# Kernel optimization log

Hardware: AMD Instinct MI355X
Metric: run time of the kernel (lower is better)

The kernel has to match this reference:

```python
import jax, jax.numpy as jnp
import numpy as np

ACTION_SCALE = 0.01
LOG_STD_MIN, LOG_STD_MAX = -20.0, 2.0


def setup_inputs() -> dict:
    key = jax.random.key(0)
    k1, k2, k3 = jax.random.split(key, 3)
    B, N, D = 8, 1024, 128
    kv = jax.random.normal(k1, (B, N, 4 * D), dtype=jnp.float32)
    positions = jax.random.normal(k2, (B, N, 3), dtype=jnp.float32)
    eps = jax.random.normal(k3, (B, N, 3), dtype=jnp.float32)  # standard-normal sample for rsample
    return {"kv": kv, "positions": positions, "eps": eps}


def reference(kv, positions, eps):
    # Split Atomwise output into mean/std key-value embeddings: each [B, N, D]
    k_mu, v_mu, k_sigma, v_sigma = jnp.split(kv, 4, axis=-1)

    # Low-rank attention-like pairwise scores: [B, N, N]
    rel_shifts_mean = jnp.einsum("bid,bjd->bij", k_mu, v_mu)
    rel_shifts_log_std = jnp.einsum("bid,bjd->bij", k_sigma, v_sigma)

    # All-pairs unit displacement vectors: [B, N, N, 3]
    P = positions[:, :, None, :] - positions[:, None, :, :]
    norm = jnp.linalg.norm(P, axis=-1) + 1e-8
    P = P / norm[..., None]

    # Weighted sum over the j axis (torch dim=-2): [B, N, 3]
    actions_mean = jnp.einsum("bijc,bij->bic", P, rel_shifts_mean)
    actions_log_std = jnp.clip(
        jnp.einsum("bijc,bij->bic", P, rel_shifts_log_std), LOG_STD_MIN, LOG_STD_MAX
    )
    actions_std = jnp.exp(actions_log_std)

    # TanhNormal rsample (training branch) with externally supplied noise eps
    pre_tanh = actions_mean + actions_std * eps
    actions = jnp.tanh(pre_tanh)

    # Normal log-prob minus tanh log-det-Jacobian
    normal_lp = (
        -0.5 * ((pre_tanh - actions_mean) / actions_std) ** 2
        - actions_log_std
        - 0.5 * jnp.log(2.0 * jnp.pi)
    )
    log_det = (
        2.0 * jnp.log(2.0)
        + jax.nn.log_sigmoid(2.0 * pre_tanh)
        + jax.nn.log_sigmoid(-2.0 * pre_tanh)
    )
    log_prob = jnp.sum(normal_lp - log_det, axis=(1, 2))[:, None]  # [B, 1]

    actions = actions * ACTION_SCALE
    # change-of-variables correction for the action_scale factor
    n_dims = pre_tanh.shape[1] * pre_tanh.shape[2]
    log_prob = log_prob - n_dims * jnp.log(ACTION_SCALE)
    return actions, log_prob
```

## Files before the change

### kernel.cpp

```cpp
#include <hip/hip_runtime.h>
#include <math.h>


#define NTOK 1024
#define LPCONST 14147.0828114f

typedef __bf16 bf16x8 __attribute__((ext_vector_type(8)));
typedef float f32x4 __attribute__((ext_vector_type(4)));
#define MFMA(a, b, c) __builtin_amdgcn_mfma_f32_16x16x32_bf16(a, b, c, 0, 0, 0)

__device__ __forceinline__ unsigned short to_bf16(float x) {
    return (unsigned short)((__float_as_uint(x) + 0x8000u) >> 16);
}

template <int CTRL>
__device__ __forceinline__ float dpp_add(float v) {
    int y = __builtin_amdgcn_update_dpp(0, __float_as_int(v), CTRL, 0xf, 0xf, true);
    return v + __int_as_float(y);
}
__device__ __forceinline__ float red16(float v) {
    v = dpp_add<0xB1>(v);
    v = dpp_add<0x4E>(v);
    v = dpp_add<0x141>(v);
    v = dpp_add<0x140>(v);
    return v;
}

__device__ __forceinline__ float softplusf(float z) {
    return z > 20.f ? z : log1pf(expf(z));
}

__global__ __launch_bounds__(256) void prepass_kernel(
    const float* __restrict__ kv, unsigned short* __restrict__ frag,
    float* __restrict__ out)
{
    const int t = blockIdx.x * 256 + threadIdx.x;
    if (t < 8) out[8 * NTOK * 3 + t] = LPCONST;

    const int lane = t & 63;
    const int kc   = (t >> 6) & 3;
    const int tile = (t >> 8) & 63;
    const int b    = (t >> 14) & 7;
    const int side = t >> 17;

    const int row = tile * 16 + (lane & 15);
    const int kof = kc * 32 + (lane >> 4) * 8;
    const float* gp = kv + ((size_t)b * NTOK + row) * 512 + side * 128 + kof;
    const float4 m0 = *(const float4*)gp;
    const float4 m1 = *(const float4*)(gp + 4);
    const float4 s0 = *(const float4*)(gp + 256);
    const float4 s1 = *(const float4*)(gp + 260);

    unsigned short* cp = frag + (size_t)side * 2097152 +
                         (size_t)(b * 64 + tile) * 4096 + kc * 1024 + lane * 8;
    ushort4 h0, h1;
    h0.x = to_bf16(m0.x); h0.y = to_bf16(m0.y); h0.z = to_bf16(m0.z); h0.w = to_bf16(m0.w);
    h1.x = to_bf16(m1.x); h1.y = to_bf16(m1.y); h1.z = to_bf16(m1.z); h1.w = to_bf16(m1.w);
    *(ushort4*)(cp + 0) = h0; *(ushort4*)(cp + 4) = h1;
    h0.x = to_bf16(s0.x); h0.y = to_bf16(s0.y); h0.z = to_bf16(s0.z); h0.w = to_bf16(s0.w);
    h1.x = to_bf16(s1.x); h1.y = to_bf16(s1.y); h1.z = to_bf16(s1.z); h1.w = to_bf16(s1.w);
    *(ushort4*)(cp + 512) = h0; *(ushort4*)(cp + 516) = h1;
}

__global__ __launch_bounds__(512) void actor_kernel(
    const unsigned short* __restrict__ frag, const float* __restrict__ pos,
    const float* __restrict__ eps, float* __restrict__ out)
{
    const int t = threadIdx.x;
    const int w = t >> 6;
    const int lane = t & 63;
    const int q = lane >> 4;
    const int r16 = lane & 15;
    const int b   = blockIdx.x & 7;
    const int itx = blockIdx.x >> 3;
    const int i0 = itx * 16;

    const unsigned short* fragK = frag;
    const unsigned short* fragV = frag + 2097152;
    const float* posb = pos + (size_t)b * NTOK * 3;

    __shared__ float spos[NTOK * 3];
    __shared__ float wacc[8 * 16 * 6];
    __shared__ float fin[96];

    #pragma unroll
    for (int u = t; u < 768; u += 512)
        *(float4*)&spos[u * 4] = *(const float4*)&posb[u * 4];

    const unsigned short* kp = fragK + (size_t)(b * 64 + itx) * 4096 + lane * 8;
    bf16x8 Km[4], Ks[4];
    #pragma unroll
    for (int kc = 0; kc < 4; ++kc) {
        Km[kc] = *(const bf16x8*)(kp + kc * 1024);
        Ks[kc] = *(const bf16x8*)(kp + kc * 1024 + 512);
    }

    __syncthreads();

    const int i = i0 + r16;
    const float pix = spos[i * 3 + 0];
    const float piy = spos[i * 3 + 1];
    const float piz = spos[i * 3 + 2];

    float am0 = 0.f, am1 = 0.f, am2 = 0.f;
    float al0 = 0.f, al1 = 0.f, al2 = 0.f;

    const unsigned short* vbase =
        fragV + (size_t)(b * 64 + w * 8) * 4096 + lane * 8;

    #pragma unroll 2
    for (int jt = 0; jt < 8; ++jt) {
        const unsigned short* vp = vbase + jt * 4096;
        f32x4 accm = (f32x4){0.f, 0.f, 0.f, 0.f};
        f32x4 accs = (f32x4){0.f, 0.f, 0.f, 0.f};
        #pragma unroll
        for (int kc = 0; kc < 4; ++kc) {
            const bf16x8 Vm = *(const bf16x8*)(vp + kc * 1024);
            const bf16x8 Vs = *(const bf16x8*)(vp + kc * 1024 + 512);
            accm = MFMA(Vm, Km[kc], accm);
            accs = MFMA(Vs, Ks[kc], accs);
        }
        const int jbase = (w * 8 + jt) * 16 + q * 4;
        #pragma unroll
        for (int reg = 0; reg < 4; ++reg) {
            const float* pj = &spos[(jbase + reg) * 3];
            const float dx = pix - pj[0];
            const float dy = piy - pj[1];
            const float dz = piz - pj[2];
            const float d2 = dx * dx + dy * dy + dz * dz;
            const float inv = d2 > 0.f ? rsqrtf(d2) : 0.f;
            const float wm = accm[reg] * inv;
            const float ws = accs[reg] * inv;
            am0 = fmaf(dx, wm, am0); am1 = fmaf(dy, wm, am1); am2 = fmaf(dz, wm, am2);
            al0 = fmaf(dx, ws, al0); al1 = fmaf(dy, ws, al1); al2 = fmaf(dz, ws, al2);
        }
    }

    am0 += __shfl_xor(am0, 16, 64); am0 += __shfl_xor(am0, 32, 64);
    am1 += __shfl_xor(am1, 16, 64); am1 += __shfl_xor(am1, 32, 64);
    am2 += __shfl_xor(am2, 16, 64); am2 += __shfl_xor(am2, 32, 64);
    al0 += __shfl_xor(al0, 16, 64); al0 += __shfl_xor(al0, 32, 64);
    al1 += __shfl_xor(al1, 16, 64); al1 += __shfl_xor(al1, 32, 64);
    al2 += __shfl_xor(al2, 16, 64); al2 += __shfl_xor(al2, 32, 64);

    if (lane < 16) {
        float* p = wacc + (w * 16 + r16) * 6;
        p[0] = am0; p[1] = am1; p[2] = am2; p[3] = al0; p[4] = al1; p[5] = al2;
    }
    __syncthreads();
    if (t < 96) {
        float v = 0.f;
        #pragma unroll
        for (int ww = 0; ww < 8; ++ww) v += wacc[ww * 96 + t];
        fin[t] = v;
    }
    __syncthreads();

    if (t < 16) {
        const int gi = b * NTOK + i0 + t;
        const float* v = fin + t * 6;
        float lp = 0.f;
        #pragma unroll
        for (int c = 0; c < 3; ++c) {
            const float als = fminf(fmaxf(v[3 + c], -20.f), 2.f);
            const float sd = expf(als);
            const float e = eps[gi * 3 + c];
            const float pre = fmaf(sd, e, v[c]);
            out[gi * 3 + c] = tanhf(pre) * 0.01f;
            const float t2 = 2.f * pre;
            lp += -0.5f * e * e - als - 2.3052328944f + softplusf(t2) + softplusf(-t2);
        }
        lp = red16(lp);
        if (t == 0) atomicAdd(out + 8 * NTOK * 3 + b, lp);
    }
}

extern "C" void kernel_launch(void* const* d_in, const int* in_sizes, int n_in,
                              void* d_out, int out_size, void* d_ws, size_t ws_size,
                              hipStream_t stream) {
    const float* kv = (const float*)d_in[0];
    const float* pos = (const float*)d_in[1];
    const float* eps = (const float*)d_in[2];
    float* out = (float*)d_out;
    unsigned short* frag = (unsigned short*)d_ws;

    prepass_kernel<<<dim3(1024), 256, 0, stream>>>(kv, frag, out);
    actor_kernel<<<dim3(512), 512, 0, stream>>>(frag, pos, eps, out);
}
```

Before: 92.72 us.

## Process two 16-row i-tiles per block, staging K fragments in LDS

Each block now handles 32 query rows (two MFMA i-tiles) with 1024 threads across 16 waves. Each V fragment loaded from global memory is reused for two K tiles, halving V traffic per output row, and the grid shrinks to 256 blocks. K fragments are staged in shared memory instead of registers. The trade-offs are fewer blocks than CUs on the device, repeated LDS reads of K inside the inner loop, and a larger cross-wave reduction.

```diff
diff --git a/kernel.cpp b/kernel.cpp
--- a/kernel.cpp
+++ b/kernel.cpp
@@ -62,7 +62,7 @@
     *(ushort4*)(cp + 512) = h0; *(ushort4*)(cp + 516) = h1;
 }
 
-__global__ __launch_bounds__(512) void actor_kernel(
+__global__ __launch_bounds__(1024) void actor_kernel(
     const unsigned short* __restrict__ frag, const float* __restrict__ pos,
     const float* __restrict__ eps, float* __restrict__ out)
 {
@@ -71,92 +71,127 @@
     const int lane = t & 63;
     const int q = lane >> 4;
     const int r16 = lane & 15;
-    const int b   = blockIdx.x & 7;
-    const int itx = blockIdx.x >> 3;
-    const int i0 = itx * 16;
+    const int b    = blockIdx.x & 7;
+    const int ithx = blockIdx.x >> 3;
+    const int i0 = ithx * 32;
 
     const unsigned short* fragK = frag;
     const unsigned short* fragV = frag + 2097152;
     const float* posb = pos + (size_t)b * NTOK * 3;
 
+    __shared__ unsigned short sK[8192];
     __shared__ float spos[NTOK * 3];
-    __shared__ float wacc[8 * 16 * 6];
-    __shared__ float fin[96];
+    __shared__ float wacc[16 * 32 * 6];
+    __shared__ float fin[192];
+
+    {
+        const unsigned short* kg =
+            fragK + (size_t)(b * 64 + ithx * 2) * 4096 + t * 8;
+        *(ushort4*)&sK[t * 8 + 0] = *(const ushort4*)(kg + 0);
+        *(ushort4*)&sK[t * 8 + 4] = *(const ushort4*)(kg + 4);
+    }
+    if (t < 768) *(float4*)&spos[t * 4] = *(const float4*)&posb[t * 4];
+    __syncthreads();
+
+    const float pix0 = spos[(i0 + r16) * 3 + 0];
+    const float piy0 = spos[(i0 + r16) * 3 + 1];
+    const float piz0 = spos[(i0 + r16) * 3 + 2];
+    const float pix1 = spos[(i0 + 16 + r16) * 3 + 0];
+    const float piy1 = spos[(i0 + 16 + r16) * 3 + 1];
+    const float piz1 = spos[(i0 + 16 + r16) * 3 + 2];
+
+    float am[2][3] = {};
+    float al[2][3] = {};
+
+    const unsigned short* vbase =
+        fragV + (size_t)(b * 64 + w * 4) * 4096 + lane * 8;
+    const int klofs = lane * 8;
 
     #pragma unroll
-    for (int u = t; u < 768; u += 512)
-        *(float4*)&spos[u * 4] = *(const float4*)&posb[u * 4];
-
-    const unsigned short* kp = fragK + (size_t)(b * 64 + itx) * 4096 + lane * 8;
-    bf16x8 Km[4], Ks[4];
-    #pragma unroll
-    for (int kc = 0; kc < 4; ++kc) {
-        Km[kc] = *(const bf16x8*)(kp + kc * 1024);
-        Ks[kc] = *(const bf16x8*)(kp + kc * 1024 + 512);
-    }
-
-    __syncthreads();
-
-    const int i = i0 + r16;
-    const float pix = spos[i * 3 + 0];
-    const float piy = spos[i * 3 + 1];
-    const float piz = spos[i * 3 + 2];
-
-    float am0 = 0.f, am1 = 0.f, am2 = 0.f;
-    float al0 = 0.f, al1 = 0.f, al2 = 0.f;
-
-    const unsigned short* vbase =
-        fragV + (size_t)(b * 64 + w * 8) * 4096 + lane * 8;
-
-    #pragma unroll 2
-    for (int jt = 0; jt < 8; ++jt) {
+    for (int jt = 0; jt < 4; ++jt) {
         const unsigned short* vp = vbase + jt * 4096;
-        f32x4 accm = (f32x4){0.f, 0.f, 0.f, 0.f};
-        f32x4 accs = (f32x4){0.f, 0.f, 0.f, 0.f};
+        f32x4 accm0 = (f32x4){0.f, 0.f, 0.f, 0.f};
+        f32x4 accs0 = (f32x4){0.f, 0.f, 0.f, 0.f};
+        f32x4 accm1 = (f32x4){0.f, 0.f, 0.f, 0.f};
+        f32x4 accs1 = (f32x4){0.f, 0.f, 0.f, 0.f};
         #pragma unroll
         for (int kc = 0; kc < 4; ++kc) {
             const bf16x8 Vm = *(const bf16x8*)(vp + kc * 1024);
             const bf16x8 Vs = *(const bf16x8*)(vp + kc * 1024 + 512);
-            accm = MFMA(Vm, Km[kc], accm);
-            accs = MFMA(Vs, Ks[kc], accs);
-        }
-        const int jbase = (w * 8 + jt) * 16 + q * 4;
+            const bf16x8 K0m = *(const bf16x8*)&sK[kc * 1024 + klofs];
+            const bf16x8 K0s = *(const bf16x8*)&sK[kc * 1024 + 512 + klofs];
+            const bf16x8 K1m = *(const bf16x8*)&sK[4096 + kc * 1024 + klofs];
+            const bf16x8 K1s = *(const bf16x8*)&sK[4096 + kc * 1024 + 512 + klofs];
+            accm0 = MFMA(Vm, K0m, accm0);
+            accs0 = MFMA(Vs, K0s, accs0);
+            accm1 = MFMA(Vm, K1m, accm1);
+            accs1 = MFMA(Vs, K1s, accs1);
+        }
+        const int jbase = (w * 4 + jt) * 16 + q * 4;
         #pragma unroll
         for (int reg = 0; reg < 4; ++reg) {
             const float* pj = &spos[(jbase + reg) * 3];
-            const float dx = pix - pj[0];
-            const float dy = piy - pj[1];
-            const float dz = piz - pj[2];
-            const float d2 = dx * dx + dy * dy + dz * dz;
-            const float inv = d2 > 0.f ? rsqrtf(d2) : 0.f;
-            const float wm = accm[reg] * inv;
-            const float ws = accs[reg] * inv;
-            am0 = fmaf(dx, wm, am0); am1 = fmaf(dy, wm, am1); am2 = fmaf(dz, wm, am2);
-            al0 = fmaf(dx, ws, al0); al1 = fmaf(dy, ws, al1); al2 = fmaf(dz, ws, al2);
-        }
-    }
-
-    am0 += __shfl_xor(am0, 16, 64); am0 += __shfl_xor(am0, 32, 64);
-    am1 += __shfl_xor(am1, 16, 64); am1 += __shfl_xor(am1, 32, 64);
-    am2 += __shfl_xor(am2, 16, 64); am2 += __shfl_xor(am2, 32, 64);
-    al0 += __shfl_xor(al0, 16, 64); al0 += __shfl_xor(al0, 32, 64);
-    al1 += __shfl_xor(al1, 16, 64); al1 += __shfl_xor(al1, 32, 64);
-    al2 += __shfl_xor(al2, 16, 64); al2 += __shfl_xor(al2, 32, 64);
+            {
+                const float dx = pix0 - pj[0];
+                const float dy = piy0 - pj[1];
+                const float dz = piz0 - pj[2];
+                const float d2 = dx * dx + dy * dy + dz * dz;
+                const float inv = d2 > 0.f ? rsqrtf(d2) : 0.f;
+                const float wm = accm0[reg] * inv;
+                const float ws = accs0[reg] * inv;
+                am[0][0] = fmaf(dx, wm, am[0][0]);
+                am[0][1] = fmaf(dy, wm, am[0][1]);
+                am[0][2] = fmaf(dz, wm, am[0][2]);
+                al[0][0] = fmaf(dx, ws, al[0][0]);
+                al[0][1] = fmaf(dy, ws, al[0][1]);
+                al[0][2] = fmaf(dz, ws, al[0][2]);
+            }
+            {
+                const float dx = pix1 - pj[0];
+                const float dy = piy1 - pj[1];
+                const float dz = piz1 - pj[2];
+                const float d2 = dx * dx + dy * dy + dz * dz;
+                const float inv = d2 > 0.f ? rsqrtf(d2) : 0.f;
+                const float wm = accm1[reg] * inv;
+                const float ws = accs1[reg] * inv;
+                am[1][0] = fmaf(dx, wm, am[1][0]);
+                am[1][1] = fmaf(dy, wm, am[1][1]);
+                am[1][2] = fmaf(dz, wm, am[1][2]);
+                al[1][0] = fmaf(dx, ws, al[1][0]);
+                al[1][1] = fmaf(dy, ws, al[1][1]);
+                al[1][2] = fmaf(dz, ws, al[1][2]);
+            }
+        }
+    }
+
+    #pragma unroll
+    for (int tile = 0; tile < 2; ++tile)
+        #pragma unroll
+        for (int c = 0; c < 3; ++c) {
+            float vm = am[tile][c], vl = al[tile][c];
+            vm += __shfl_xor(vm, 16, 64); vm += __shfl_xor(vm, 32, 64);
+            vl += __shfl_xor(vl, 16, 64); vl += __shfl_xor(vl, 32, 64);
+            am[tile][c] = vm; al[tile][c] = vl;
+        }
 
     if (lane < 16) {
-        float* p = wacc + (w * 16 + r16) * 6;
-        p[0] = am0; p[1] = am1; p[2] = am2; p[3] = al0; p[4] = al1; p[5] = al2;
+        #pragma unroll
+        for (int tile = 0; tile < 2; ++tile) {
+            float* p = wacc + (w * 32 + tile * 16 + r16) * 6;
+            p[0] = am[tile][0]; p[1] = am[tile][1]; p[2] = am[tile][2];
+            p[3] = al[tile][0]; p[4] = al[tile][1]; p[5] = al[tile][2];
+        }
     }
     __syncthreads();
-    if (t < 96) {
+    if (t < 192) {
         float v = 0.f;
         #pragma unroll
-        for (int ww = 0; ww < 8; ++ww) v += wacc[ww * 96 + t];
+        for (int ww = 0; ww < 16; ++ww) v += wacc[ww * 192 + t];
         fin[t] = v;
     }
     __syncthreads();
 
-    if (t < 16) {
+    if (t < 32) {
         const int gi = b * NTOK + i0 + t;
         const float* v = fin + t * 6;
         float lp = 0.f;
@@ -171,6 +206,7 @@
             lp += -0.5f * e * e - als - 2.3052328944f + softplusf(t2) + softplusf(-t2);
         }
         lp = red16(lp);
+        lp += __shfl_xor(lp, 16, 64);
         if (t == 0) atomicAdd(out + 8 * NTOK * 3 + b, lp);
     }
 }
@@ -185,5 +221,5 @@
     unsigned short* frag = (unsigned short*)d_ws;
 
     prepass_kernel<<<dim3(1024), 256, 0, stream>>>(kv, frag, out);
-    actor_kernel<<<dim3(512), 512, 0, stream>>>(frag, pos, eps, out);
-}
+    actor_kernel<<<dim3(256), 1024, 0, stream>>>(frag, pos, eps, out);
+}
```

Result: slower. 109.4 us (+18.0%).
